# Performance work log

Hardware: AMD Instinct MI355X
Metric: run time of the kernel (lower is better)

## Reference

```python
import jax, jax.numpy as jnp
import numpy as np

N, C, K, H = 131072, 512, 128, 8  # points, channels, patch_size, heads


def setup_inputs() -> dict:
    key = jax.random.key(0)
    ks = jax.random.split(key, 6)
    feat = jax.random.normal(ks[0], (N, C), dtype=jnp.float32)
    Wqkv = jax.random.normal(ks[1], (C, 3 * C), dtype=jnp.float32) * 0.02
    bqkv = jax.random.normal(ks[2], (3 * C,), dtype=jnp.float32) * 0.02
    Wproj = jax.random.normal(ks[3], (C, C), dtype=jnp.float32) * 0.02
    bproj = jax.random.normal(ks[4], (C,), dtype=jnp.float32) * 0.02
    order = jax.random.permutation(ks[5], N).astype(jnp.int64)  # serialized order (all clusters full)
    inverse = jnp.argsort(order).astype(jnp.int64)              # serialized inverse
    return {"feat": feat, "Wqkv": Wqkv, "bqkv": bqkv, "Wproj": Wproj,
            "bproj": bproj, "order": order, "inverse": inverse}


def reference(feat, Wqkv, bqkv, Wproj, bproj, order, inverse):
    hd = C // H
    scale = hd ** -0.5
    qkv = feat @ Wqkv + bqkv                 # [N, 3C]
    qkv = qkv[order]                         # gather by serialized order
    qkv = qkv.reshape(-1, K, 3, H, hd)       # [W, K, 3, H, hd]
    qkv = jnp.moveaxis(qkv, 2, 0)            # [3, W, K, H, hd]
    q = jnp.swapaxes(qkv[0], 1, 2)           # [W, H, K, hd]
    k = jnp.swapaxes(qkv[1], 1, 2)
    v = jnp.swapaxes(qkv[2], 1, 2)
    # upcast_attention / upcast_softmax -> compute scores & softmax in fp32
    attn = jnp.einsum('whkd,whjd->whkj', (q * scale).astype(jnp.float32),
                      k.astype(jnp.float32))             # [W, H, K, K]
    attn = jax.nn.softmax(attn, axis=-1).astype(feat.dtype)
    out = jnp.einsum('whkj,whjd->whkd', attn, v)          # [W, H, K, hd]
    out = jnp.swapaxes(out, 1, 2).reshape(-1, C)          # [N, C]
    out = out[inverse]                                    # scatter back via inverse
    out = out @ Wproj + bproj
    return out
```

## Files before the change

### kernel.cpp

```cpp
#include <hip/hip_runtime.h>
#include <hip/hip_bf16.h>
#include <cstdint>
#include <cstddef>

typedef __bf16 bf16;
typedef __bf16 bf16x8 __attribute__((ext_vector_type(8)));
typedef float f32x4 __attribute__((ext_vector_type(4)));

#define N_PTS 131072
#define CDIM  512
#define C3    1536
#define HD    64
#define NH    8
#define KWIN  128

static __device__ __forceinline__ bf16 cvt(float x) { return (bf16)x; }

static __device__ __forceinline__ void gld16(const bf16* g, bf16* l) {
    __builtin_amdgcn_global_load_lds(
        (const __attribute__((address_space(1))) void*)g,
        (__attribute__((address_space(3))) void*)l, 16, 0, 0);
}

__global__ __launch_bounds__(256) void k_prep(
    const float* __restrict__ Wqkv, const float* __restrict__ Wproj,
    bf16* __restrict__ Wqkv_t, bf16* __restrict__ Wproj_t)
{
    int idx = blockIdx.x * 256 + threadIdx.x;
    if (idx < CDIM * C3) {
        int k = idx / C3, c = idx % C3;
        Wqkv_t[(size_t)c * CDIM + k] = cvt(Wqkv[idx]);
    } else {
        int j = idx - CDIM * C3;
        if (j < CDIM * CDIM) {
            int k = j / CDIM, c = j % CDIM;
            Wproj_t[(size_t)c * CDIM + k] = cvt(Wproj[j]);
        }
    }
}

__global__ __launch_bounds__(256) void k_gather(
    const float* __restrict__ feat, const int* __restrict__ order,
    bf16* __restrict__ feat_g)
{
    int row = blockIdx.x * 2 + (threadIdx.x >> 7);
    int c   = (threadIdx.x & 127) << 2;
    int src = order[row];
    float4 v = *reinterpret_cast<const float4*>(feat + (size_t)src * CDIM + c);
    union { bf16 e[4]; uint2 u; } pk;
    pk.e[0] = cvt(v.x); pk.e[1] = cvt(v.y); pk.e[2] = cvt(v.z); pk.e[3] = cvt(v.w);
    *reinterpret_cast<uint2*>(feat_g + (size_t)row * CDIM + c) = pk.u;
}

template <int NT>
__global__ __launch_bounds__(512) void k_gemm8(
    const bf16* __restrict__ Ag, const bf16* __restrict__ Bt,
    const float* __restrict__ bias, bf16* __restrict__ outp)
{
    __shared__ __align__(16) bf16 As[2][256 * 64];
    __shared__ __align__(16) bf16 Bs[2][256 * 64];

    const int t    = threadIdx.x;
    const int lane = t & 63;
    const int wv   = t >> 6;
    const int wr   = wv >> 2;
    const int wc   = wv & 3;
    const int g    = lane >> 4, r16 = lane & 15;

    const int nwg = gridDim.x;
    const int bid = blockIdx.x;
    const int swz = (bid & 7) * (nwg >> 3) + (bid >> 3);
    const int m0  = (swz / NT) * 256;
    const int n0  = (swz % NT) * 256;

    const int NKT = CDIM / 64;

    int aSrc[2][2], bSrc[2][2], dstE[2][2];
#pragma unroll
    for (int h = 0; h < 2; ++h)
#pragma unroll
        for (int j = 0; j < 2; ++j) {
            int L = wv * 128 + j * 64 + lane;
            int row_l = L >> 3, p8 = L & 7;
            int s8 = (p8 - (row_l & 7)) & 7;
            int grow = h * 128 + row_l;
            aSrc[h][j] = (m0 + grow) * CDIM + s8 * 8;
            bSrc[h][j] = (n0 + grow) * CDIM + s8 * 8;
            dstE[h][j] = h * 8192 + (wv * 128 + j * 64) * 8;
        }

    int aoff[2][2][4];
    int boff[2][4];
#pragma unroll
    for (int grp = 0; grp < 2; ++grp)
#pragma unroll
        for (int kh = 0; kh < 2; ++kh)
#pragma unroll
            for (int q = 0; q < 4; ++q) {
                int row = wr * 128 + (grp * 4 + q) * 16 + r16;
                aoff[grp][kh][q] = row * 128 +
                    (((kh * 4 + g + (r16 & 7)) & 7) << 4);
            }
#pragma unroll
    for (int kh = 0; kh < 2; ++kh)
#pragma unroll
        for (int n = 0; n < 4; ++n) {
            int row = wc * 64 + n * 16 + r16;
            boff[kh][n] = row * 128 +
                (((kh * 4 + g + (r16 & 7)) & 7) << 4);
        }

    f32x4 acc[8][4];
    const f32x4 z = {0.f, 0.f, 0.f, 0.f};
#pragma unroll
    for (int i = 0; i < 8; ++i)
#pragma unroll
        for (int n = 0; n < 4; ++n) acc[i][n] = z;

    bf16x8 afr[2][4], bfr[2][4];

    auto stageA = [&](int tau) {
        const int b = tau & 1, ko = tau * 64;
#pragma unroll
        for (int h = 0; h < 2; ++h)
#pragma unroll
            for (int j = 0; j < 2; ++j)
                gld16(Ag + aSrc[h][j] + ko, &As[b][dstE[h][j]]);
    };
    auto stageB = [&](int tau) {
        const int b = tau & 1, ko = tau * 64;
#pragma unroll
        for (int h = 0; h < 2; ++h)
#pragma unroll
            for (int j = 0; j < 2; ++j)
                gld16(Bt + bSrc[h][j] + ko, &Bs[b][dstE[h][j]]);
    };
    auto readA = [&](int set, int b, int grp, int kh) {
        const char* ab = reinterpret_cast<const char*>(&As[b][0]);
#pragma unroll
        for (int q = 0; q < 4; ++q)
            afr[set][q] = *reinterpret_cast<const bf16x8*>(ab + aoff[grp][kh][q]);
    };
    auto readB = [&](int b, int kh) {
        const char* bb = reinterpret_cast<const char*>(&Bs[b][0]);
#pragma unroll
        for (int n = 0; n < 4; ++n)
            bfr[kh][n] = *reinterpret_cast<const bf16x8*>(bb + boff[kh][n]);
    };

    stageB(0); stageA(0); stageB(1); stageA(1);
    asm volatile("s_waitcnt vmcnt(8)" ::: "memory");
    __builtin_amdgcn_s_barrier();
    readA(0, 0, 0, 0);
    readB(0, 0);
    asm volatile("s_waitcnt lgkmcnt(0)" ::: "memory");
    __builtin_amdgcn_sched_barrier(0);

#pragma unroll
    for (int tau = 0; tau < NKT; ++tau) {
#pragma unroll
        for (int p = 0; p < 4; ++p) {
            const int pi  = tau * 4 + p;
            const int grp = p & 1, kh = p >> 1;

            if (p == 2 && tau + 2 < NKT) stageB(tau + 2);
            if (p == 3 && tau + 2 < NKT) stageA(tau + 2);

            if (pi + 1 < NKT * 4) {
                const int pn   = (p + 1) & 3;
                const int taun = tau + (p == 3);
                const int bn   = taun & 1;
                readA((pi + 1) & 1, bn, pn & 1, pn >> 1);
                if (pn == 0 || pn == 2) readB(bn, pn >> 1);
            }

            __builtin_amdgcn_s_setprio(1);
#pragma unroll
            for (int q = 0; q < 4; ++q)
#pragma unroll
                for (int n = 0; n < 4; ++n)
                    acc[grp * 4 + q][n] = __builtin_amdgcn_mfma_f32_16x16x32_bf16(
                        afr[pi & 1][q], bfr[kh][n], acc[grp * 4 + q][n], 0, 0, 0);
            __builtin_amdgcn_s_setprio(0);

            asm volatile("s_waitcnt lgkmcnt(0)" ::: "memory");
            __builtin_amdgcn_sched_barrier(0);
            if (p == 2) {
                if (tau + 2 < NKT)
                    asm volatile("s_waitcnt vmcnt(4)" ::: "memory");
                else
                    asm volatile("s_waitcnt vmcnt(0)" ::: "memory");
            }
            __builtin_amdgcn_s_barrier();
        }
    }

    const int ldo = NT * 256;
#pragma unroll
    for (int n = 0; n < 4; ++n) {
        int col = n0 + wc * 64 + n * 16 + r16;
        float b = bias[col];
#pragma unroll
        for (int i = 0; i < 8; ++i)
#pragma unroll
            for (int j = 0; j < 4; ++j) {
                int row = m0 + wr * 128 + i * 16 + g * 4 + j;
                outp[(size_t)row * ldo + col] = cvt(acc[i][n][j] + b);
            }
    }
}

__global__ __launch_bounds__(512) void k_attn_proj(
    const bf16* __restrict__ qkv_s, const bf16* __restrict__ Wp_t,
    const float* __restrict__ bproj, const int* __restrict__ order,
    float* __restrict__ out)
{
    __shared__ __align__(16) char smem[138240];
    __shared__ int ord_s[KWIN];
    bf16 (*Q)[72]   = reinterpret_cast<bf16 (*)[72]>(smem);
    bf16 (*Kt)[72]  = reinterpret_cast<bf16 (*)[72]>(smem + 18432);
    bf16 (*P)[136]  = reinterpret_cast<bf16 (*)[136]>(smem);
    bf16 (*Vt)[136] = reinterpret_cast<bf16 (*)[136]>(smem + 36864);
    bf16 (*Oh)[72]  = reinterpret_cast<bf16 (*)[72]>(smem + 54272);
    bf16* Wp        = reinterpret_cast<bf16*>(smem + 72704);

    const int t    = threadIdx.x;
    const int lane = t & 63;
    const int wv   = t >> 6;
    const int g    = lane >> 4, r16 = lane & 15;
    const int w    = blockIdx.x;

    if (t < KWIN) ord_s[t] = order[w * KWIN + t];

    int wpRow[4], wpSlot[4];
#pragma unroll
    for (int q4 = 0; q4 < 4; ++q4) {
        int L = q4 * 512 + t;
        wpRow[q4]  = L >> 2;
        wpSlot[q4] = ((L & 3) - (wpRow[q4] >> 1)) & 3;
    }

    int paoff[4];
#pragma unroll
    for (int ci = 0; ci < 4; ++ci) {
        int row = wv * 64 + ci * 16 + r16;
        paoff[ci] = row * 64 + (((g + (row >> 1)) & 3) << 4);
    }

    f32x4 pacc[4][8];
    const f32x4 z = {0.f, 0.f, 0.f, 0.f};
#pragma unroll
    for (int ci = 0; ci < 4; ++ci)
#pragma unroll
        for (int qi = 0; qi < 8; ++qi) pacc[ci][qi] = z;

    const float scale = 0.125f;

    for (int h = 0; h < NH; ++h) {
        const bf16* base = qkv_s + (size_t)w * KWIN * C3 + h * HD;
#pragma unroll
        for (int it = 0; it < 2; ++it) {
            int s   = it * 512 + t;
            int tok = s >> 3;
            int c8  = (s & 7) << 3;
            size_t roff = (size_t)tok * C3 + c8;
            *reinterpret_cast<uint4*>(&Q[tok][c8])  =
                *reinterpret_cast<const uint4*>(base + roff);
            *reinterpret_cast<uint4*>(&Kt[tok][c8]) =
                *reinterpret_cast<const uint4*>(base + roff + CDIM);
            uint4 vvec = *reinterpret_cast<const uint4*>(base + roff + 2 * CDIM);
            const bf16* ve = reinterpret_cast<const bf16*>(&vvec);
#pragma unroll
            for (int i = 0; i < 8; ++i) Vt[c8 + i][tok] = ve[i];
        }
#pragma unroll
        for (int ks = 0; ks < 2; ++ks)
#pragma unroll
            for (int q4 = 0; q4 < 4; ++q4) {
                gld16(Wp_t + (size_t)wpRow[q4] * CDIM + h * HD + ks * 32
                          + wpSlot[q4] * 8,
                      Wp + ks * 16384 + (q4 * 512 + wv * 64) * 8);
            }
        __syncthreads();

        f32x4 sc[8];
#pragma unroll
        for (int n = 0; n < 8; ++n) sc[n] = z;
#pragma unroll
        for (int ks = 0; ks < 2; ++ks) {
            bf16x8 aq = *reinterpret_cast<const bf16x8*>(
                &Q[wv * 16 + r16][ks * 32 + g * 8]);
#pragma unroll
            for (int n = 0; n < 8; ++n) {
                bf16x8 bk = *reinterpret_cast<const bf16x8*>(
                    &Kt[n * 16 + r16][ks * 32 + g * 8]);
                sc[n] = __builtin_amdgcn_mfma_f32_16x16x32_bf16(
                    aq, bk, sc[n], 0, 0, 0);
            }
        }

        float inv_sum[4];
#pragma unroll
        for (int j = 0; j < 4; ++j) {
            float mx = -3.0e38f;
#pragma unroll
            for (int n = 0; n < 8; ++n) mx = fmaxf(mx, sc[n][j]);
            mx = fmaxf(mx, __shfl_xor(mx, 1));
            mx = fmaxf(mx, __shfl_xor(mx, 2));
            mx = fmaxf(mx, __shfl_xor(mx, 4));
            mx = fmaxf(mx, __shfl_xor(mx, 8));
            mx *= scale;
            float ssum = 0.f;
#pragma unroll
            for (int n = 0; n < 8; ++n) {
                float p = __expf(sc[n][j] * scale - mx);
                sc[n][j] = p;
                ssum += p;
            }
            ssum += __shfl_xor(ssum, 1);
            ssum += __shfl_xor(ssum, 2);
            ssum += __shfl_xor(ssum, 4);
            ssum += __shfl_xor(ssum, 8);
            inv_sum[j] = 1.f / ssum;
        }

        __syncthreads();

#pragma unroll
        for (int n = 0; n < 8; ++n)
#pragma unroll
            for (int j = 0; j < 4; ++j)
                P[wv * 16 + g * 4 + j][n * 16 + r16] =
                    cvt(sc[n][j] * inv_sum[j]);

        f32x4 o[4];
#pragma unroll
        for (int n = 0; n < 4; ++n) o[n] = z;
#pragma unroll
        for (int kt = 0; kt < 4; ++kt) {
            bf16x8 ap = *reinterpret_cast<const bf16x8*>(
                &P[wv * 16 + r16][kt * 32 + g * 8]);
#pragma unroll
            for (int n = 0; n < 4; ++n) {
                bf16x8 bvv = *reinterpret_cast<const bf16x8*>(
                    &Vt[n * 16 + r16][kt * 32 + g * 8]);
                o[n] = __builtin_amdgcn_mfma_f32_16x16x32_bf16(
                    ap, bvv, o[n], 0, 0, 0);
            }
        }

#pragma unroll
        for (int n = 0; n < 4; ++n)
#pragma unroll
            for (int j = 0; j < 4; ++j)
                Oh[wv * 16 + g * 4 + j][n * 16 + r16] = cvt(o[n][j]);

        __syncthreads();

#pragma unroll
        for (int ks = 0; ks < 2; ++ks) {
            const char* wb = reinterpret_cast<const char*>(Wp + ks * 16384);
            bf16x8 af[4], bq[8];
#pragma unroll
            for (int ci = 0; ci < 4; ++ci)
                af[ci] = *reinterpret_cast<const bf16x8*>(wb + paoff[ci]);
#pragma unroll
            for (int qi = 0; qi < 8; ++qi)
                bq[qi] = *reinterpret_cast<const bf16x8*>(
                    &Oh[qi * 16 + r16][ks * 32 + g * 8]);
            __builtin_amdgcn_s_setprio(1);
#pragma unroll
            for (int ci = 0; ci < 4; ++ci)
#pragma unroll
                for (int qi = 0; qi < 8; ++qi)
                    pacc[ci][qi] = __builtin_amdgcn_mfma_f32_16x16x32_bf16(
                        af[ci], bq[qi], pacc[ci][qi], 0, 0, 0);
            __builtin_amdgcn_s_setprio(0);
        }
        __syncthreads();
    }

#pragma unroll
    for (int ci = 0; ci < 4; ++ci) {
        int c0 = wv * 64 + ci * 16 + g * 4;
        float4 bp = *reinterpret_cast<const float4*>(bproj + c0);
#pragma unroll
        for (int qi = 0; qi < 8; ++qi) {
            int q = qi * 16 + r16;
            float4 v;
            v.x = pacc[ci][qi][0] + bp.x;
            v.y = pacc[ci][qi][1] + bp.y;
            v.z = pacc[ci][qi][2] + bp.z;
            v.w = pacc[ci][qi][3] + bp.w;
            *reinterpret_cast<float4*>(
                out + (size_t)ord_s[q] * CDIM + c0) = v;
        }
    }
}

extern "C" void kernel_launch(void* const* d_in, const int* in_sizes, int n_in,
                              void* d_out, int out_size, void* d_ws, size_t ws_size,
                              hipStream_t stream)
{
    const float* feat    = (const float*)d_in[0];
    const float* Wqkv    = (const float*)d_in[1];
    const float* bqkv    = (const float*)d_in[2];
    const float* Wproj   = (const float*)d_in[3];
    const float* bproj   = (const float*)d_in[4];
    const int*   order   = (const int*)d_in[5];
    float* out = (float*)d_out;

    const size_t qkv_bytes = (size_t)N_PTS * C3 * sizeof(bf16);
    const size_t gat_bytes = (size_t)N_PTS * CDIM * sizeof(bf16);
    const size_t wq_bytes  = (size_t)C3 * CDIM * sizeof(bf16);
    const size_t wp_bytes  = (size_t)CDIM * CDIM * sizeof(bf16);
    if (ws_size < qkv_bytes + gat_bytes + wq_bytes + wp_bytes) return;

    bf16* qkv_s   = (bf16*)d_ws;
    bf16* feat_g  = (bf16*)((char*)d_ws + qkv_bytes);
    bf16* Wqkv_t  = (bf16*)((char*)d_ws + qkv_bytes + gat_bytes);
    bf16* Wproj_t = (bf16*)((char*)d_ws + qkv_bytes + gat_bytes + wq_bytes);

    k_prep<<<dim3((CDIM * C3 + CDIM * CDIM + 255) / 256), 256, 0, stream>>>(
        Wqkv, Wproj, Wqkv_t, Wproj_t);
    k_gather<<<dim3(N_PTS / 2), 256, 0, stream>>>(feat, order, feat_g);
    k_gemm8<C3 / 256><<<dim3((N_PTS / 256) * (C3 / 256)), 512, 0, stream>>>(
        feat_g, Wqkv_t, bqkv, qkv_s);
    k_attn_proj<<<dim3(N_PTS / KWIN), 512, 0, stream>>>(
        qkv_s, Wproj_t, bproj, order, out);
}
```

Measured before the change: 662.8 us.

## Double-buffer per-head Q/K/V staging and read Wproj fragments directly from global

Restructures the fused attention+projection kernel so the next head's Q/K are fetched into a second LDS buffer with async global-to-LDS loads, and its V is loaded into registers and transposed into a second buffer, all while the current head computes. The LDS staging of Wproj is removed; each wave loads its projection A-fragments straight from global memory into registers. An XOR-style swizzle (rotation) replaces row padding for Q/K and V to avoid bank conflicts, and one barrier per head is dropped. It raises LDS use to about 150KB and adds register pressure from the prefetched V and weight fragments.

```diff
diff --git a/kernel.cpp b/kernel.cpp
--- a/kernel.cpp
+++ b/kernel.cpp
@@ -20,6 +20,21 @@
     __builtin_amdgcn_global_load_lds(
         (const __attribute__((address_space(1))) void*)g,
         (__attribute__((address_space(3))) void*)l, 16, 0, 0);
+}
+
+static __device__ __forceinline__ uint4 rot128(uint4 u, int r) {
+    uint32_t x = u.x, y = u.y, z = u.z, w = u.w;
+    uint32_t x1 = (x >> 16) | (y << 16), y1 = (y >> 16) | (z << 16),
+             z1 = (z >> 16) | (w << 16), w1 = (w >> 16) | (x << 16);
+    bool o1 = r & 1;
+    x = o1 ? x1 : x; y = o1 ? y1 : y; z = o1 ? z1 : z; w = o1 ? w1 : w;
+    bool o2 = r & 2;
+    uint32_t t0 = x;
+    x = o2 ? y : x; y = o2 ? z : y; z = o2 ? w : z; w = o2 ? t0 : w;
+    bool o4 = r & 4;
+    uint32_t tx = x, ty = y;
+    x = o4 ? z : x; y = o4 ? w : y; z = o4 ? tx : z; w = o4 ? ty : w;
+    uint4 o; o.x = x; o.y = y; o.z = z; o.w = w; return o;
 }
 
 __global__ __launch_bounds__(256) void k_prep(
@@ -215,14 +230,14 @@
     const float* __restrict__ bproj, const int* __restrict__ order,
     float* __restrict__ out)
 {
-    __shared__ __align__(16) char smem[138240];
+    __shared__ __align__(16) char smem[153600];
     __shared__ int ord_s[KWIN];
-    bf16 (*Q)[72]   = reinterpret_cast<bf16 (*)[72]>(smem);
-    bf16 (*Kt)[72]  = reinterpret_cast<bf16 (*)[72]>(smem + 18432);
-    bf16 (*P)[136]  = reinterpret_cast<bf16 (*)[136]>(smem);
-    bf16 (*Vt)[136] = reinterpret_cast<bf16 (*)[136]>(smem + 36864);
-    bf16 (*Oh)[72]  = reinterpret_cast<bf16 (*)[72]>(smem + 54272);
-    bf16* Wp        = reinterpret_cast<bf16*>(smem + 72704);
+    bf16* Qb = reinterpret_cast<bf16*>(smem);
+    bf16* Kb = reinterpret_cast<bf16*>(smem + 32768);
+    unsigned short* Vtu = reinterpret_cast<unsigned short*>(smem + 65536);
+    const bf16* Vtb = reinterpret_cast<const bf16*>(smem + 65536);
+    bf16 (*P)[136] = reinterpret_cast<bf16 (*)[136]>(smem + 100352);
+    bf16 (*Oh)[72] = reinterpret_cast<bf16 (*)[72]>(smem + 135168);
 
     const int t    = threadIdx.x;
     const int lane = t & 63;
@@ -232,20 +247,52 @@
 
     if (t < KWIN) ord_s[t] = order[w * KWIN + t];
 
-    int wpRow[4], wpSlot[4];
-#pragma unroll
-    for (int q4 = 0; q4 < 4; ++q4) {
-        int L = q4 * 512 + t;
-        wpRow[q4]  = L >> 2;
-        wpSlot[q4] = ((L & 3) - (wpRow[q4] >> 1)) & 3;
-    }
-
-    int paoff[4];
-#pragma unroll
-    for (int ci = 0; ci < 4; ++ci) {
-        int row = wv * 64 + ci * 16 + r16;
-        paoff[ci] = row * 64 + (((g + (row >> 1)) & 3) << 4);
-    }
+    const bf16* base = qkv_s + (size_t)w * KWIN * C3;
+
+    int qsrc[2], qdst[2];
+#pragma unroll
+    for (int j = 0; j < 2; ++j) {
+        int L = t + j * 512;
+        int row = L >> 3, p = L & 7, s = (p - row) & 7;
+        qsrc[j] = row * C3 + s * 8;
+        qdst[j] = j * 4096 + wv * 512;
+    }
+    auto stageQK = [&](int hh) {
+        const int b = hh & 1;
+#pragma unroll
+        for (int j = 0; j < 2; ++j) {
+            gld16(base + hh * HD + qsrc[j],        Qb + b * 8192 + qdst[j]);
+            gld16(base + CDIM + hh * HD + qsrc[j], Kb + b * 8192 + qdst[j]);
+        }
+    };
+
+    const int vtok = t >> 3;
+    const int vd0  = (t & 7) * 8;
+    const int vr   = t & 7;
+    int vaddr[8];
+#pragma unroll
+    for (int k = 0; k < 8; ++k)
+        vaddr[k] = (vd0 + ((k + vr) & 7)) * 136 + vtok;
+
+    auto loadV = [&](int hh, uint4& ua, uint4& ub) {
+        const float* dummy = nullptr; (void)dummy;
+        ua = *reinterpret_cast<const uint4*>(
+            base + (size_t)vtok * C3 + 2 * CDIM + hh * HD + vd0);
+        ub = *reinterpret_cast<const uint4*>(
+            base + (size_t)(vtok + 64) * C3 + 2 * CDIM + hh * HD + vd0);
+    };
+    auto packV = [&](int hh, uint4 ua, uint4 ub) {
+        const int b = hh & 1;
+        uint4 ra = rot128(ua, vr), rb = rot128(ub, vr);
+        uint32_t wa[4] = {ra.x, ra.y, ra.z, ra.w};
+        uint32_t wb[4] = {rb.x, rb.y, rb.z, rb.w};
+        unsigned short* vt = Vtu + b * 8704;
+#pragma unroll
+        for (int k = 0; k < 8; ++k) {
+            vt[vaddr[k]]      = (unsigned short)(wa[k >> 1] >> ((k & 1) * 16));
+            vt[vaddr[k] + 64] = (unsigned short)(wb[k >> 1] >> ((k & 1) * 16));
+        }
+    };
 
     f32x4 pacc[4][8];
     const f32x4 z = {0.f, 0.f, 0.f, 0.f};
@@ -256,44 +303,35 @@
 
     const float scale = 0.125f;
 
+    {
+        stageQK(0);
+        uint4 ua, ub;
+        loadV(0, ua, ub);
+        packV(0, ua, ub);
+        __syncthreads();
+    }
+
     for (int h = 0; h < NH; ++h) {
-        const bf16* base = qkv_s + (size_t)w * KWIN * C3 + h * HD;
-#pragma unroll
-        for (int it = 0; it < 2; ++it) {
-            int s   = it * 512 + t;
-            int tok = s >> 3;
-            int c8  = (s & 7) << 3;
-            size_t roff = (size_t)tok * C3 + c8;
-            *reinterpret_cast<uint4*>(&Q[tok][c8])  =
-                *reinterpret_cast<const uint4*>(base + roff);
-            *reinterpret_cast<uint4*>(&Kt[tok][c8]) =
-                *reinterpret_cast<const uint4*>(base + roff + CDIM);
-            uint4 vvec = *reinterpret_cast<const uint4*>(base + roff + 2 * CDIM);
-            const bf16* ve = reinterpret_cast<const bf16*>(&vvec);
-#pragma unroll
-            for (int i = 0; i < 8; ++i) Vt[c8 + i][tok] = ve[i];
-        }
-#pragma unroll
-        for (int ks = 0; ks < 2; ++ks)
-#pragma unroll
-            for (int q4 = 0; q4 < 4; ++q4) {
-                gld16(Wp_t + (size_t)wpRow[q4] * CDIM + h * HD + ks * 32
-                          + wpSlot[q4] * 8,
-                      Wp + ks * 16384 + (q4 * 512 + wv * 64) * 8);
-            }
-        __syncthreads();
+        const int qb = h & 1;
+        uint4 vA, vB;
+        if (h < NH - 1) {
+            stageQK(h + 1);
+            loadV(h + 1, vA, vB);
+        }
 
         f32x4 sc[8];
 #pragma unroll
         for (int n = 0; n < 8; ++n) sc[n] = z;
 #pragma unroll
         for (int ks = 0; ks < 2; ++ks) {
+            int qrow = wv * 16 + r16;
             bf16x8 aq = *reinterpret_cast<const bf16x8*>(
-                &Q[wv * 16 + r16][ks * 32 + g * 8]);
+                Qb + qb * 8192 + qrow * 64 + (((ks * 4 + g) + qrow) & 7) * 8);
 #pragma unroll
             for (int n = 0; n < 8; ++n) {
+                int krow = n * 16 + r16;
                 bf16x8 bk = *reinterpret_cast<const bf16x8*>(
-                    &Kt[n * 16 + r16][ks * 32 + g * 8]);
+                    Kb + qb * 8192 + krow * 64 + (((ks * 4 + g) + krow) & 7) * 8);
                 sc[n] = __builtin_amdgcn_mfma_f32_16x16x32_bf16(
                     aq, bk, sc[n], 0, 0, 0);
             }
@@ -324,8 +362,6 @@
             inv_sum[j] = 1.f / ssum;
         }
 
-        __syncthreads();
-
 #pragma unroll
         for (int n = 0; n < 8; ++n)
 #pragma unroll
@@ -333,6 +369,15 @@
                 P[wv * 16 + g * 4 + j][n * 16 + r16] =
                     cvt(sc[n][j] * inv_sum[j]);
 
+        bf16x8 af[2][4];
+#pragma unroll
+        for (int ks = 0; ks < 2; ++ks)
+#pragma unroll
+            for (int ci = 0; ci < 4; ++ci)
+                af[ks][ci] = *reinterpret_cast<const bf16x8*>(
+                    Wp_t + (size_t)(wv * 64 + ci * 16 + r16) * CDIM
+                         + h * HD + ks * 32 + g * 8);
+
         f32x4 o[4];
 #pragma unroll
         for (int n = 0; n < 4; ++n) o[n] = z;
@@ -343,12 +388,14 @@
 #pragma unroll
             for (int n = 0; n < 4; ++n) {
                 bf16x8 bvv = *reinterpret_cast<const bf16x8*>(
-                    &Vt[n * 16 + r16][kt * 32 + g * 8]);
+                    Vtb + qb * 8704 + (n * 16 + r16) * 136 + kt * 32 + g * 8);
                 o[n] = __builtin_amdgcn_mfma_f32_16x16x32_bf16(
                     ap, bvv, o[n], 0, 0, 0);
             }
         }
 
+        if (h < NH - 1) packV(h + 1, vA, vB);
+
 #pragma unroll
         for (int n = 0; n < 4; ++n)
 #pragma unroll
@@ -359,22 +406,16 @@
 
 #pragma unroll
         for (int ks = 0; ks < 2; ++ks) {
-            const char* wb = reinterpret_cast<const char*>(Wp + ks * 16384);
-            bf16x8 af[4], bq[8];
-#pragma unroll
-            for (int ci = 0; ci < 4; ++ci)
-                af[ci] = *reinterpret_cast<const bf16x8*>(wb + paoff[ci]);
-#pragma unroll
-            for (int qi = 0; qi < 8; ++qi)
-                bq[qi] = *reinterpret_cast<const bf16x8*>(
+            __builtin_amdgcn_s_setprio(1);
+#pragma unroll
+            for (int qi = 0; qi < 8; ++qi) {
+                bf16x8 bq = *reinterpret_cast<const bf16x8*>(
                     &Oh[qi * 16 + r16][ks * 32 + g * 8]);
-            __builtin_amdgcn_s_setprio(1);
-#pragma unroll
-            for (int ci = 0; ci < 4; ++ci)
-#pragma unroll
-                for (int qi = 0; qi < 8; ++qi)
+#pragma unroll
+                for (int ci = 0; ci < 4; ++ci)
                     pacc[ci][qi] = __builtin_amdgcn_mfma_f32_16x16x32_bf16(
-                        af[ci], bq[qi], pacc[ci][qi], 0, 0, 0);
+                        af[ks][ci], bq, pacc[ci][qi], 0, 0, 0);
+            }
             __builtin_amdgcn_s_setprio(0);
         }
         __syncthreads();
```

Measured after the change: 653.9 us. Within noise of the previous version (-1.3%).
